# Kernel optimization log

Hardware: AMD Instinct MI355X
Metric: run time of the kernel (lower is better)

## Reference

```python
import jax, jax.numpy as jnp
import numpy as np
import math

D = 2048
N_HEADS = 16
D_HEAD = D // N_HEADS
B = 2
L = 2048


def _rope_tables(seq_len, d_head, base=10000.0):
    # standard half-rotation RoPE tables, shape [L, d_head]
    inv_freq = 1.0 / (base ** (jnp.arange(0, d_head, 2, dtype=jnp.float32) / d_head))
    ang = jnp.arange(seq_len, dtype=jnp.float32)[:, None] * inv_freq[None, :]  # [L, d_head/2]
    cos = jnp.concatenate([jnp.cos(ang), jnp.cos(ang)], axis=-1)  # [L, d_head]
    sin = jnp.concatenate([jnp.sin(ang), jnp.sin(ang)], axis=-1)
    return cos, sin


def _apply_rope(x, cos, sin):
    # x: [B, H, L, d_head]; rotate_half convention
    half = x.shape[-1] // 2
    x_rot = jnp.concatenate([-x[..., half:], x[..., :half]], axis=-1)
    return x * cos[None, None, :, :] + x_rot * sin[None, None, :, :]


def setup_inputs() -> dict:
    key = jax.random.key(0)
    k1, k2, k3 = jax.random.split(key, 3)
    x = jax.random.normal(k1, (B, L, D), dtype=jnp.float32)
    w_qkv = jax.random.normal(k2, (D, 3 * D), dtype=jnp.float32) * (1.0 / math.sqrt(D))
    w_out = jax.random.normal(k3, (D, D), dtype=jnp.float32) * (1.0 / math.sqrt(D))
    s_qk = jnp.asarray(math.sqrt(D_HEAD), dtype=jnp.float32)  # init sqrt(d_head)
    return {"x": x, "w_qkv": w_qkv, "w_out": w_out, "s_qk": s_qk}


def reference(x, w_qkv, w_out, s_qk):
    Bs, Ls, Ds = x.shape
    qkv = jnp.einsum("bld,de->ble", x, w_qkv).reshape(Bs, Ls, 3, N_HEADS, D_HEAD)
    q, k, v = qkv[:, :, 0], qkv[:, :, 1], qkv[:, :, 2]
    # -> [B, H, L, d_head]
    q = jnp.transpose(q, (0, 2, 1, 3))
    k = jnp.transpose(k, (0, 2, 1, 3))
    v = jnp.transpose(v, (0, 2, 1, 3))
    cos, sin = _rope_tables(Ls, D_HEAD)
    q = _apply_rope(q, cos, sin)
    k = _apply_rope(k, cos, sin)
    # L2-normalize per head (torch F.normalize eps=1e-12)
    q = q / jnp.maximum(jnp.linalg.norm(q, axis=-1, keepdims=True), 1e-12)
    k = k / jnp.maximum(jnp.linalg.norm(k, axis=-1, keepdims=True), 1e-12)
    # softmax((q*s_qk) @ k^T) with causal mask, scale=1.0
    scores = jnp.einsum("bhqd,bhkd->bhqk", q * s_qk, k)
    causal = jnp.tril(jnp.ones((Ls, Ls), dtype=bool))
    scores = jnp.where(causal[None, None, :, :], scores, -jnp.inf)
    attn = jax.nn.softmax(scores, axis=-1)
    out = jnp.einsum("bhqk,bhkd->bhqd", attn, v)
    out = jnp.transpose(out, (0, 2, 1, 3)).reshape(Bs, Ls, Ds)
    return jnp.einsum("bld,de->ble", out, w_out)
```

## Files before the change

### kernel.cpp

```cpp
#include <hip/hip_runtime.h>
#include <math.h>


#define D 2048
#define NH 16
#define DH 128
#define BB 2
#define LL 2048
#define BHD (BB*NH)
#define MROWS (BB*LL)
#define KDIM D

typedef __attribute__((ext_vector_type(8))) short short8;
typedef __attribute__((ext_vector_type(4))) float floatx4;

__device__ __forceinline__ unsigned short f2bf(float f) {
    unsigned u = __float_as_uint(f);
    unsigned r = u + 0x7FFFu + ((u >> 16) & 1u);
    return (unsigned short)(r >> 16);
}
__device__ __forceinline__ float bf2f(unsigned short u) {
    return __uint_as_float(((unsigned)u) << 16);
}

__device__ __forceinline__ void async16(const void* g, void* lds) {
    __builtin_amdgcn_global_load_lds(
        (const __attribute__((address_space(1))) unsigned int*)g,
        (__attribute__((address_space(3))) unsigned int*)lds, 16, 0, 0);
}

template<int CTRL>
__device__ __forceinline__ float dpp_movf(float x) {
    return __int_as_float(__builtin_amdgcn_update_dpp(
        0, __float_as_int(x), CTRL, 0xF, 0xF, true));
}
__device__ __forceinline__ float row_max16(float x) {
    x = fmaxf(x, dpp_movf<0xB1>(x));
    x = fmaxf(x, dpp_movf<0x4E>(x));
    x = fmaxf(x, dpp_movf<0x124>(x));
    x = fmaxf(x, dpp_movf<0x128>(x));
    return x;
}
__device__ __forceinline__ float row_sum16(float x) {
    x += dpp_movf<0xB1>(x);
    x += dpp_movf<0x4E>(x);
    x += dpp_movf<0x124>(x);
    x += dpp_movf<0x128>(x);
    return x;
}

__global__ __launch_bounds__(256)
void cast_bf16_kernel_v2(const float* __restrict__ in,
                         unsigned short* __restrict__ out, int n4)
{
    int i = blockIdx.x * 256 + threadIdx.x;
    if (i < n4) {
        float4 v = ((const float4*)in)[i];
        ushort4 o;
        o.x = f2bf(v.x); o.y = f2bf(v.y); o.z = f2bf(v.z); o.w = f2bf(v.w);
        ((ushort4*)out)[i] = o;
    }
}

__global__ __launch_bounds__(256)
void transpose_cast_kernel_v2(const float* __restrict__ W,
                              unsigned short* __restrict__ Wt, int K, int N)
{
    __shared__ float tile[32][33];
    const int tx = threadIdx.x & 31, ty = threadIdx.x >> 5;
    const int n0 = blockIdx.x * 32, k0 = blockIdx.y * 32;
#pragma unroll
    for (int r = 0; r < 4; r++)
        tile[ty + 8 * r][tx] = W[(size_t)(k0 + ty + 8 * r) * N + n0 + tx];
    __syncthreads();
#pragma unroll
    for (int r = 0; r < 4; r++)
        Wt[(size_t)(n0 + ty + 8 * r) * K + k0 + tx] = f2bf(tile[tx][ty + 8 * r]);
}

__global__ __launch_bounds__(256)
void transpose_v_kernel_v2(const unsigned short* __restrict__ Vb,
                           unsigned short* __restrict__ VtG)
{
    __shared__ unsigned short tile[32][34];
    const int tx = threadIdx.x & 31, ty = threadIdx.x >> 5;
    const int l0 = blockIdx.x * 32, d0 = blockIdx.y * 32;
    const int bh = blockIdx.z;
    const unsigned short* src = Vb + (size_t)bh * LL * DH;
    unsigned short* dst = VtG + (size_t)bh * DH * LL;
#pragma unroll
    for (int r = 0; r < 4; r++)
        tile[ty + 8 * r][tx] = src[(size_t)(l0 + ty + 8 * r) * DH + d0 + tx];
    __syncthreads();
#pragma unroll
    for (int r = 0; r < 4; r++)
        dst[(size_t)(d0 + ty + 8 * r) * LL + l0 + tx] = tile[tx][ty + 8 * r];
}

template<int N, int MODE>
__global__ __launch_bounds__(256)
void mfma_gemm_v2(const unsigned short* __restrict__ A,
                  const unsigned short* __restrict__ Bt,
                  float* __restrict__ C, unsigned short* __restrict__ Qo,
                  unsigned short* __restrict__ Ko, unsigned short* __restrict__ Vo)
{
    __shared__ unsigned short As[128 * 32];
    __shared__ unsigned short Bs[128 * 32];
    const int t = threadIdx.x;
    const int w = t >> 6, lane = t & 63;
    const int lrow = lane & 15, quad = lane >> 4;
    const int m0 = blockIdx.y * 128, n0 = blockIdx.x * 128;
    const int wm = (w >> 1) * 64, wn = (w & 1) * 64;

    floatx4 acc[4][4];
#pragma unroll
    for (int i = 0; i < 4; i++)
#pragma unroll
        for (int j = 0; j < 4; j++) acc[i][j] = (floatx4){0.f, 0.f, 0.f, 0.f};

    const int srow = 32 * w + (lane >> 2);
    const int sseg = (lane & 3) * 8;

    for (int k0 = 0; k0 < KDIM; k0 += 32) {
        __syncthreads();
        async16(&A [(size_t)(m0 + srow)      * KDIM + k0 + sseg], &As[(32 * w)      * 32]);
        async16(&A [(size_t)(m0 + srow + 16) * KDIM + k0 + sseg], &As[(32 * w + 16) * 32]);
        async16(&Bt[(size_t)(n0 + srow)      * KDIM + k0 + sseg], &Bs[(32 * w)      * 32]);
        async16(&Bt[(size_t)(n0 + srow + 16) * KDIM + k0 + sseg], &Bs[(32 * w + 16) * 32]);
        __syncthreads();

        short8 a[4], b[4];
#pragma unroll
        for (int i = 0; i < 4; i++)
            a[i] = *(const short8*)&As[(wm + i * 16 + lrow) * 32 + quad * 8];
#pragma unroll
        for (int j = 0; j < 4; j++)
            b[j] = *(const short8*)&Bs[(wn + j * 16 + lrow) * 32 + quad * 8];
#pragma unroll
        for (int i = 0; i < 4; i++)
#pragma unroll
            for (int j = 0; j < 4; j++)
                acc[i][j] = __builtin_amdgcn_mfma_f32_16x16x32_bf16(a[i], b[j], acc[i][j], 0, 0, 0);
    }

    if (MODE == 0) {
#pragma unroll
        for (int i = 0; i < 4; i++)
#pragma unroll
            for (int j = 0; j < 4; j++) {
                int col = n0 + wn + j * 16 + lrow;
#pragma unroll
                for (int r = 0; r < 4; r++) {
                    int m = m0 + wm + i * 16 + quad * 4 + r;
                    C[(size_t)m * N + col] = acc[i][j][r];
                }
            }
    } else {
        const int s = n0 >> 11;
        const int h = (n0 & 2047) >> 7;
        unsigned short* dst = (s == 0) ? Qo : (s == 1) ? Ko : Vo;
#pragma unroll
        for (int i = 0; i < 4; i++)
#pragma unroll
            for (int j = 0; j < 4; j++) {
                int dh = wn + j * 16 + lrow;
#pragma unroll
                for (int r = 0; r < 4; r++) {
                    int m = m0 + wm + i * 16 + quad * 4 + r;
                    int b = m >> 11, l = m & 2047;
                    dst[(((size_t)b * NH + h) * LL + l) * DH + dh] = f2bf(acc[i][j][r]);
                }
            }
    }
}

__global__ __launch_bounds__(128)
void rope_norm_kernel_v2(unsigned short* __restrict__ Q,
                         unsigned short* __restrict__ K,
                         const float* __restrict__ s_qk_ptr)
{
    const int l  = blockIdx.x;
    const int bh = blockIdx.y;
    const int d  = threadIdx.x;
    __shared__ float sh[128];

    const size_t base = ((size_t)bh * LL + l) * DH + d;
    float qv = bf2f(Q[base]);
    float kv = bf2f(K[base]);

    const int i = d & 63;
    float ang = (float)l * expf(-0.14391157f * (float)i);
    float c = cosf(ang), s = sinf(ang);

    sh[d] = qv; __syncthreads();
    float qrot = (d < 64) ? -sh[d + 64] : sh[d - 64];
    float qr = fmaf(qv, c, qrot * s);
    __syncthreads();

    sh[d] = kv; __syncthreads();
    float krot = (d < 64) ? -sh[d + 64] : sh[d - 64];
    float kr = fmaf(kv, c, krot * s);
    __syncthreads();

    sh[d] = qr * qr; __syncthreads();
    for (int st = 64; st > 0; st >>= 1) {
        if (d < st) sh[d] += sh[d + st];
        __syncthreads();
    }
    float qn = sqrtf(sh[0]);
    __syncthreads();

    sh[d] = kr * kr; __syncthreads();
    for (int st = 64; st > 0; st >>= 1) {
        if (d < st) sh[d] += sh[d + st];
        __syncthreads();
    }
    float kn = sqrtf(sh[0]);

    float sqk = s_qk_ptr[0];
    Q[base] = f2bf(qr / fmaxf(qn, 1e-12f) * sqk);
    K[base] = f2bf(kr / fmaxf(kn, 1e-12f));
}

#define ABQ 128
#define ABK 64
__global__ __launch_bounds__(256, 2)
void attn_mfma_kernel_v5(const unsigned short* __restrict__ Q,
                         const unsigned short* __restrict__ K,
                         const unsigned short* __restrict__ Vt,
                         unsigned short* __restrict__ AOb)
{
    __shared__ __align__(16) unsigned short Ks[2][ABK * DH];
    __shared__ __align__(16) unsigned short Vs[2][DH * ABK];
    __shared__ __align__(16) unsigned short Ps[4][32][64];

    const int t = threadIdx.x;
    const int w = t >> 6, lane = t & 63;
    const int lrow = lane & 15, quad = lane >> 4;
    const int bh = blockIdx.x;
    const int y  = blockIdx.y;
    const int qt = (y < 8) ? (15 - y) : (y - 8);
    const int q0 = qt * ABQ;
    const int qw = q0 + w * 32;

    const unsigned short* Qb = Q  + (size_t)bh * LL * DH;
    const unsigned short* Kb = K  + (size_t)bh * LL * DH;
    const unsigned short* Vg = Vt + (size_t)bh * DH * LL;

    short8 aq[2][4];
#pragma unroll
    for (int h = 0; h < 2; h++)
#pragma unroll
        for (int kk = 0; kk < 4; kk++)
            aq[h][kk] = *(const short8*)&Qb[(size_t)(qw + 16 * h + lrow) * DH
                                            + kk * 32 + quad * 8];

    floatx4 oacc[2][8];
#pragma unroll
    for (int h = 0; h < 2; h++)
#pragma unroll
        for (int dt = 0; dt < 8; dt++) oacc[h][dt] = (floatx4){0.f, 0.f, 0.f, 0.f};
    float mrow[2][4], lsum[2][4];
#pragma unroll
    for (int h = 0; h < 2; h++)
#pragma unroll
        for (int r = 0; r < 4; r++) { mrow[h][r] = -1e30f; lsum[h][r] = 0.f; }

    auto STAGE = [&](int tile, int buf) {
        const int k0s = tile * ABK;
#pragma unroll
        for (int c = 0; c < 4; c++) {
            int row = 16 * w + 4 * c;
            int r   = row + (lane >> 4);
            int col = (lane & 15) ^ (r & 7);
            async16(&Kb[(size_t)(k0s + r) * DH + col * 8], &Ks[buf][row * DH]);
        }
#pragma unroll
        for (int c = 0; c < 4; c++) {
            int row = 32 * w + 8 * c;
            int r   = row + (lane >> 3);
            int col = (lane & 7) ^ (r & 7);
            async16(&Vg[(size_t)r * LL + k0s + col * 8], &Vs[buf][row * ABK]);
        }
    };

    const int ntiles = 2 * qt + 2;
    STAGE(0, 0);
    __syncthreads();

    int cur = 0;
    for (int tile = 0; tile < ntiles; tile++) {
        const int k0 = tile * ABK;
        if (tile + 1 < ntiles) STAGE(tile + 1, cur ^ 1);

        floatx4 sacc[2][4];
#pragma unroll
        for (int h = 0; h < 2; h++)
#pragma unroll
            for (int j = 0; j < 4; j++) sacc[h][j] = (floatx4){0.f, 0.f, 0.f, 0.f};
        __builtin_amdgcn_s_setprio(1);
#pragma unroll
        for (int kk = 0; kk < 4; kk++) {
#pragma unroll
            for (int j = 0; j < 4; j++) {
                int slot = (kk * 4 + quad) ^ (lrow & 7);
                short8 bk = *(const short8*)&Ks[cur][(j * 16 + lrow) * DH + slot * 8];
                sacc[0][j] = __builtin_amdgcn_mfma_f32_16x16x32_bf16(aq[0][kk], bk, sacc[0][j], 0, 0, 0);
                sacc[1][j] = __builtin_amdgcn_mfma_f32_16x16x32_bf16(aq[1][kk], bk, sacc[1][j], 0, 0, 0);
            }
        }
        __builtin_amdgcn_s_setprio(0);

#pragma unroll
        for (int h = 0; h < 2; h++) {
            if (k0 + ABK - 1 > qw + 16 * h) {
#pragma unroll
                for (int j = 0; j < 4; j++) {
                    int key = k0 + j * 16 + lrow;
#pragma unroll
                    for (int r = 0; r < 4; r++) {
                        int q = qw + 16 * h + quad * 4 + r;
                        if (key > q) sacc[h][j][r] = -1e30f;
                    }
                }
            }
        }

#pragma unroll
        for (int h = 0; h < 2; h++) {
            float alpha[4];
#pragma unroll
            for (int r = 0; r < 4; r++) {
                float mt = fmaxf(fmaxf(sacc[h][0][r], sacc[h][1][r]),
                                 fmaxf(sacc[h][2][r], sacc[h][3][r]));
                mt = row_max16(mt);
                float mn = fmaxf(mrow[h][r], mt);
                alpha[r] = __expf(mrow[h][r] - mn);
                mrow[h][r] = mn;
            }
#pragma unroll
            for (int r = 0; r < 4; r++) {
                int rowp = 16 * h + quad * 4 + r;
                float rs = 0.f;
#pragma unroll
                for (int j = 0; j < 4; j++) {
                    float p = __expf(sacc[h][j][r] - mrow[h][r]);
                    rs += p;
                    int slot = (2 * j + (lrow >> 3)) ^ (rowp & 7);
                    Ps[w][rowp][slot * 8 + (lrow & 7)] = f2bf(p);
                }
                rs = row_sum16(rs);
                lsum[h][r] = lsum[h][r] * alpha[r] + rs;
            }
#pragma unroll
            for (int dt = 0; dt < 8; dt++)
#pragma unroll
                for (int r = 0; r < 4; r++) oacc[h][dt][r] *= alpha[r];
        }

        __builtin_amdgcn_s_setprio(1);
#pragma unroll
        for (int kk2 = 0; kk2 < 2; kk2++) {
            int pslot = (kk2 * 4 + quad) ^ (lrow & 7);
            short8 pa0 = *(const short8*)&Ps[w][lrow][pslot * 8];
            short8 pa1 = *(const short8*)&Ps[w][16 + lrow][pslot * 8];
#pragma unroll
            for (int dt = 0; dt < 8; dt++) {
                int slot = (kk2 * 4 + quad) ^ (lrow & 7);
                short8 bv = *(const short8*)&Vs[cur][(dt * 16 + lrow) * ABK + slot * 8];
                oacc[0][dt] = __builtin_amdgcn_mfma_f32_16x16x32_bf16(pa0, bv, oacc[0][dt], 0, 0, 0);
                oacc[1][dt] = __builtin_amdgcn_mfma_f32_16x16x32_bf16(pa1, bv, oacc[1][dt], 0, 0, 0);
            }
        }
        __builtin_amdgcn_s_setprio(0);

        __syncthreads();
        cur ^= 1;
    }

    const int b = bh >> 4, hd = bh & 15;
#pragma unroll
    for (int h = 0; h < 2; h++)
#pragma unroll
        for (int r = 0; r < 4; r++) {
            float inv = 1.f / lsum[h][r];
            int q = qw + 16 * h + quad * 4 + r;
            size_t base = ((size_t)b * LL + q) * D + hd * DH;
#pragma unroll
            for (int dt = 0; dt < 8; dt++)
                AOb[base + dt * 16 + lrow] = f2bf(oacc[h][dt][r] * inv);
        }
}

extern "C" void kernel_launch(void* const* d_in, const int* in_sizes, int n_in,
                              void* d_out, int out_size, void* d_ws, size_t ws_size,
                              hipStream_t stream)
{
    const float* x     = (const float*)d_in[0];
    const float* w_qkv = (const float*)d_in[1];
    const float* w_out = (const float*)d_in[2];
    const float* s_qk  = (const float*)d_in[3];
    float* out = (float*)d_out;

    const size_t SZ = (size_t)BB * NH * LL * DH;
    unsigned short* u = (unsigned short*)d_ws;
    unsigned short* xb    = u;
    unsigned short* wqkvT = xb    + (size_t)MROWS * KDIM;
    unsigned short* woutT = wqkvT + (size_t)(3 * D) * KDIM;
    unsigned short* Qb    = woutT + (size_t)D * KDIM;
    unsigned short* Kb    = Qb + SZ;
    unsigned short* Vb    = Kb + SZ;
    unsigned short* VtG   = Vb + SZ;

    cast_bf16_kernel_v2<<<(MROWS * KDIM / 4 + 255) / 256, 256, 0, stream>>>(
        x, xb, MROWS * KDIM / 4);
    transpose_cast_kernel_v2<<<dim3(3 * D / 32, KDIM / 32), 256, 0, stream>>>(
        w_qkv, wqkvT, KDIM, 3 * D);
    mfma_gemm_v2<3 * D, 1><<<dim3(3 * D / 128, MROWS / 128), 256, 0, stream>>>(
        xb, wqkvT, nullptr, Qb, Kb, Vb);
    rope_norm_kernel_v2<<<dim3(LL, BHD), 128, 0, stream>>>(Qb, Kb, s_qk);
    transpose_v_kernel_v2<<<dim3(LL / 32, DH / 32, BHD), 256, 0, stream>>>(Vb, VtG);
    attn_mfma_kernel_v5<<<dim3(BHD, LL / ABQ), 256, 0, stream>>>(Qb, Kb, VtG, xb);
    transpose_cast_kernel_v2<<<dim3(D / 32, D / 32), 256, 0, stream>>>(
        w_out, woutT, D, D);
    mfma_gemm_v2<D, 0><<<dim3(D / 128, MROWS / 128), 256, 0, stream>>>(
        xb, woutT, out, nullptr, nullptr, nullptr);
}
```

Baseline: 438.5 us.

## Triple-buffer GEMM loads and use wave-level reductions in RoPE normalization

The bf16 MFMA GEMM now stages global-to-LDS tiles into three rotating buffers, prefetching two k-steps ahead. It waits with vmcnt-based barriers and raises wave priority around the MFMA block, aiming to overlap memory latency with compute instead of fully synchronizing each k-step. The RoPE+L2-norm kernel is rewritten to process one row per wavefront with two elements per lane, using shuffle/DPP reductions instead of many shared-memory barriers. The cost is triple the LDS for the GEMM, which may reduce occupancy.

Result: slower. 473.8 us (+8.1%).

```diff
diff --git a/kernel.cpp b/kernel.cpp
--- a/kernel.cpp
+++ b/kernel.cpp
@@ -99,13 +99,13 @@
 
 template<int N, int MODE>
 __global__ __launch_bounds__(256)
-void mfma_gemm_v2(const unsigned short* __restrict__ A,
+void mfma_gemm_v3(const unsigned short* __restrict__ A,
                   const unsigned short* __restrict__ Bt,
                   float* __restrict__ C, unsigned short* __restrict__ Qo,
                   unsigned short* __restrict__ Ko, unsigned short* __restrict__ Vo)
 {
-    __shared__ unsigned short As[128 * 32];
-    __shared__ unsigned short Bs[128 * 32];
+    __shared__ unsigned short As[3][128 * 32];
+    __shared__ unsigned short Bs[3][128 * 32];
     const int t = threadIdx.x;
     const int w = t >> 6, lane = t & 63;
     const int lrow = lane & 15, quad = lane >> 4;
@@ -121,26 +121,50 @@
     const int srow = 32 * w + (lane >> 2);
     const int sseg = (lane & 3) * 8;
 
+    auto STAGE = [&](int k0, int buf) {
+        async16(&A [(size_t)(m0 + srow)      * KDIM + k0 + sseg], &As[buf][(32 * w)      * 32]);
+        async16(&A [(size_t)(m0 + srow + 16) * KDIM + k0 + sseg], &As[buf][(32 * w + 16) * 32]);
+        async16(&Bt[(size_t)(n0 + srow)      * KDIM + k0 + sseg], &Bs[buf][(32 * w)      * 32]);
+        async16(&Bt[(size_t)(n0 + srow + 16) * KDIM + k0 + sseg], &Bs[buf][(32 * w + 16) * 32]);
+    };
+
+    STAGE(0, 0);
+    STAGE(32, 1);
+    asm volatile("s_waitcnt vmcnt(4)" ::: "memory");
+    __builtin_amdgcn_s_barrier();
+    __builtin_amdgcn_sched_barrier(0);
+
+    int buf = 0;
     for (int k0 = 0; k0 < KDIM; k0 += 32) {
-        __syncthreads();
-        async16(&A [(size_t)(m0 + srow)      * KDIM + k0 + sseg], &As[(32 * w)      * 32]);
-        async16(&A [(size_t)(m0 + srow + 16) * KDIM + k0 + sseg], &As[(32 * w + 16) * 32]);
-        async16(&Bt[(size_t)(n0 + srow)      * KDIM + k0 + sseg], &Bs[(32 * w)      * 32]);
-        async16(&Bt[(size_t)(n0 + srow + 16) * KDIM + k0 + sseg], &Bs[(32 * w + 16) * 32]);
-        __syncthreads();
+        if (k0 + 64 < KDIM) {
+            int nb = buf + 2; if (nb >= 3) nb -= 3;
+            STAGE(k0 + 64, nb);
+        }
 
         short8 a[4], b[4];
 #pragma unroll
         for (int i = 0; i < 4; i++)
-            a[i] = *(const short8*)&As[(wm + i * 16 + lrow) * 32 + quad * 8];
+            a[i] = *(const short8*)&As[buf][(wm + i * 16 + lrow) * 32 + quad * 8];
 #pragma unroll
         for (int j = 0; j < 4; j++)
-            b[j] = *(const short8*)&Bs[(wn + j * 16 + lrow) * 32 + quad * 8];
+            b[j] = *(const short8*)&Bs[buf][(wn + j * 16 + lrow) * 32 + quad * 8];
+        __builtin_amdgcn_s_setprio(1);
 #pragma unroll
         for (int i = 0; i < 4; i++)
 #pragma unroll
             for (int j = 0; j < 4; j++)
                 acc[i][j] = __builtin_amdgcn_mfma_f32_16x16x32_bf16(a[i], b[j], acc[i][j], 0, 0, 0);
+        __builtin_amdgcn_s_setprio(0);
+
+        if (k0 + 32 < KDIM) {
+            if (k0 + 64 < KDIM)
+                asm volatile("s_waitcnt vmcnt(4)" ::: "memory");
+            else
+                asm volatile("s_waitcnt vmcnt(0)" ::: "memory");
+            __builtin_amdgcn_s_barrier();
+            __builtin_amdgcn_sched_barrier(0);
+        }
+        buf = buf + 1; if (buf >= 3) buf -= 3;
     }
 
     if (MODE == 0) {
@@ -174,52 +198,41 @@
     }
 }
 
-__global__ __launch_bounds__(128)
-void rope_norm_kernel_v2(unsigned short* __restrict__ Q,
+__global__ __launch_bounds__(256)
+void rope_norm_kernel_v3(unsigned short* __restrict__ Q,
                          unsigned short* __restrict__ K,
                          const float* __restrict__ s_qk_ptr)
 {
-    const int l  = blockIdx.x;
-    const int bh = blockIdx.y;
-    const int d  = threadIdx.x;
-    __shared__ float sh[128];
-
-    const size_t base = ((size_t)bh * LL + l) * DH + d;
-    float qv = bf2f(Q[base]);
-    float kv = bf2f(K[base]);
-
-    const int i = d & 63;
-    float ang = (float)l * expf(-0.14391157f * (float)i);
+    const int wid  = threadIdx.x >> 6;
+    const int lane = threadIdx.x & 63;
+    const int row  = blockIdx.x * 4 + wid;
+    const int l    = row & (LL - 1);
+    const size_t base = (size_t)row * DH;
+
+    float ang = (float)l * expf(-0.14391157f * (float)lane);
     float c = cosf(ang), s = sinf(ang);
 
-    sh[d] = qv; __syncthreads();
-    float qrot = (d < 64) ? -sh[d + 64] : sh[d - 64];
-    float qr = fmaf(qv, c, qrot * s);
-    __syncthreads();
-
-    sh[d] = kv; __syncthreads();
-    float krot = (d < 64) ? -sh[d + 64] : sh[d - 64];
-    float kr = fmaf(kv, c, krot * s);
-    __syncthreads();
-
-    sh[d] = qr * qr; __syncthreads();
-    for (int st = 64; st > 0; st >>= 1) {
-        if (d < st) sh[d] += sh[d + st];
-        __syncthreads();
-    }
-    float qn = sqrtf(sh[0]);
-    __syncthreads();
-
-    sh[d] = kr * kr; __syncthreads();
-    for (int st = 64; st > 0; st >>= 1) {
-        if (d < st) sh[d] += sh[d + st];
-        __syncthreads();
-    }
-    float kn = sqrtf(sh[0]);
+    float qlo = bf2f(Q[base + lane]), qhi = bf2f(Q[base + lane + 64]);
+    float klo = bf2f(K[base + lane]), khi = bf2f(K[base + lane + 64]);
+
+    float qr_lo = fmaf(qlo, c, (-qhi) * s);
+    float qr_hi = fmaf(qhi, c,   qlo  * s);
+    float kr_lo = fmaf(klo, c, (-khi) * s);
+    float kr_hi = fmaf(khi, c,   klo  * s);
+
+    float qs = qr_lo * qr_lo + qr_hi * qr_hi;
+    float ks = kr_lo * kr_lo + kr_hi * kr_hi;
+    qs = row_sum16(qs);  ks = row_sum16(ks);
+    qs += __shfl_xor(qs, 16);  ks += __shfl_xor(ks, 16);
+    qs += __shfl_xor(qs, 32);  ks += __shfl_xor(ks, 32);
+    float qn = fmaxf(sqrtf(qs), 1e-12f);
+    float kn = fmaxf(sqrtf(ks), 1e-12f);
 
     float sqk = s_qk_ptr[0];
-    Q[base] = f2bf(qr / fmaxf(qn, 1e-12f) * sqk);
-    K[base] = f2bf(kr / fmaxf(kn, 1e-12f));
+    Q[base + lane]      = f2bf(qr_lo / qn * sqk);
+    Q[base + lane + 64] = f2bf(qr_hi / qn * sqk);
+    K[base + lane]      = f2bf(kr_lo / kn);
+    K[base + lane + 64] = f2bf(kr_hi / kn);
 }
 
 #define ABQ 128
@@ -416,13 +429,13 @@
         x, xb, MROWS * KDIM / 4);
     transpose_cast_kernel_v2<<<dim3(3 * D / 32, KDIM / 32), 256, 0, stream>>>(
         w_qkv, wqkvT, KDIM, 3 * D);
-    mfma_gemm_v2<3 * D, 1><<<dim3(3 * D / 128, MROWS / 128), 256, 0, stream>>>(
+    mfma_gemm_v3<3 * D, 1><<<dim3(3 * D / 128, MROWS / 128), 256, 0, stream>>>(
         xb, wqkvT, nullptr, Qb, Kb, Vb);
-    rope_norm_kernel_v2<<<dim3(LL, BHD), 128, 0, stream>>>(Qb, Kb, s_qk);
+    rope_norm_kernel_v3<<<dim3(BHD * LL / 4), 256, 0, stream>>>(Qb, Kb, s_qk);
     transpose_v_kernel_v2<<<dim3(LL / 32, DH / 32, BHD), 256, 0, stream>>>(Vb, VtG);
     attn_mfma_kernel_v5<<<dim3(BHD, LL / ABQ), 256, 0, stream>>>(Qb, Kb, VtG, xb);
     transpose_cast_kernel_v2<<<dim3(D / 32, D / 32), 256, 0, stream>>>(
         w_out, woutT, D, D);
-    mfma_gemm_v2<D, 0><<<dim3(D / 128, MROWS / 128), 256, 0, stream>>>(
+    mfma_gemm_v3<D, 0><<<dim3(D / 128, MROWS / 128), 256, 0, stream>>>(
         xb, woutT, out, nullptr, nullptr, nullptr);
 }
```
